# Optimization experiments

Hardware: AMD Instinct MI355X
Metric: run time of the kernel (lower is better)

## Reference

```python
import jax, jax.numpy as jnp
import numpy as np

N_NODES = 100000
N_EDGES = 1600000
IN_F = 64
HIDDEN = [64, 64, 32]


def _glorot(key, shape):
    limit = float(np.sqrt(6.0 / (shape[0] + shape[1])))
    return jax.random.uniform(key, shape, jnp.float32, -limit, limit)


def setup_inputs() -> dict:
    key = jax.random.key(0)
    ks = jax.random.split(key, 5)
    x = jax.random.normal(ks[0], (N_NODES, IN_F), jnp.float32)
    edge_index = jax.random.randint(ks[1], (2, N_EDGES), 0, N_NODES, jnp.int64)
    dims = [IN_F] + HIDDEN
    params = {}
    for i in range(len(HIDDEN)):
        params[f"W{i+1}"] = _glorot(ks[2 + i], (dims[i], dims[i + 1]))
        params[f"b{i+1}"] = jnp.zeros((dims[i + 1],), jnp.float32)
    return {"x": x, "edge_index": edge_index, **params}


def _gcn_layer(x, src, dst, norm, W, b, n):
    # PyG GCNConv: linear transform, then normalized scatter-sum aggregation, then bias
    h = x @ W                                  # [N, out]
    msg = norm[:, None] * h[src]               # gather + edge scaling, [E+N, out]
    out = jax.ops.segment_sum(msg, dst, num_segments=n)
    return out + b


def reference(x, edge_index, W1, b1, W2, b2, W3, b3):
    n = x.shape[0]
    # add self-loops (GCNConv default add_self_loops=True)
    loops = jnp.arange(n, dtype=edge_index.dtype)
    src = jnp.concatenate([edge_index[0], loops])
    dst = jnp.concatenate([edge_index[1], loops])
    # symmetric normalization: deg over destination (col), norm = d^-1/2[src]*d^-1/2[dst]
    deg = jax.ops.segment_sum(jnp.ones_like(src, x.dtype), dst, num_segments=n)
    dinv = jnp.where(deg > 0, jax.lax.rsqrt(deg), 0.0)
    norm = dinv[src] * dinv[dst]
    h = jax.nn.relu(_gcn_layer(x, src, dst, norm, W1, b1, n))
    h = jax.nn.relu(_gcn_layer(h, src, dst, norm, W2, b2, n))
    return _gcn_layer(h, src, dst, norm, W3, b3, n)
```

## Files before the change

### kernel.cpp

```cpp
#include <hip/hip_runtime.h>
#include <hip/hip_bf16.h>


#define BLOCK 256
#define NBUCKET 512
#define CHUNK 4096
#define SLOT 4608
#define MAX_NPB 256

typedef float f32x4 __attribute__((ext_vector_type(4)));

__device__ __forceinline__ float4 fma4(float s, float4 a, float4 b) {
  return make_float4(fmaf(s, a.x, b.x), fmaf(s, a.y, b.y),
                     fmaf(s, a.z, b.z), fmaf(s, a.w, b.w));
}

__device__ __forceinline__ unsigned int bf16r(float f) {
  unsigned int u = __float_as_uint(f);
  u += 0x7fffu + ((u >> 16) & 1u);
  return u >> 16;
}

__device__ __forceinline__ void acc_bf8(float4& lo, float4& hi, uint4 u) {
  lo.x += __uint_as_float(u.x << 16);
  lo.y += __uint_as_float(u.x & 0xffff0000u);
  lo.z += __uint_as_float(u.y << 16);
  lo.w += __uint_as_float(u.y & 0xffff0000u);
  hi.x += __uint_as_float(u.z << 16);
  hi.y += __uint_as_float(u.z & 0xffff0000u);
  hi.z += __uint_as_float(u.w << 16);
  hi.w += __uint_as_float(u.w & 0xffff0000u);
}


__global__ __launch_bounds__(BLOCK) void binning_kernel(
    const int* __restrict__ src, const int* __restrict__ dst,
    int* __restrict__ bcursor, int* __restrict__ binned, int e, int npb) {
  __shared__ int h[NBUCKET];
  __shared__ int base[NBUCKET];
  for (int i = threadIdx.x; i < NBUCKET; i += BLOCK) h[i] = 0;
  __syncthreads();
  const int cbase = blockIdx.x * CHUNK;
#pragma unroll
  for (int k = 0; k < CHUNK; k += BLOCK * 4) {
    int i = cbase + k + threadIdx.x * 4;
    if (i + 3 < e) {
      int4 d4 = *(const int4*)(dst + i);
      atomicAdd(&h[d4.x / npb], 1);
      atomicAdd(&h[d4.y / npb], 1);
      atomicAdd(&h[d4.z / npb], 1);
      atomicAdd(&h[d4.w / npb], 1);
    } else {
      for (int t = 0; t < 4; ++t)
        if (i + t < e) atomicAdd(&h[dst[i + t] / npb], 1);
    }
  }
  __syncthreads();
  for (int i = threadIdx.x; i < NBUCKET; i += BLOCK) {
    int c = h[i];
    base[i] = c ? atomicAdd(&bcursor[i], c) : 0;
    h[i] = 0;
  }
  __syncthreads();
#pragma unroll
  for (int k = 0; k < CHUNK; k += BLOCK * 4) {
    int i = cbase + k + threadIdx.x * 4;
    if (i + 3 < e) {
      int4 d4 = *(const int4*)(dst + i);
      int4 s4 = *(const int4*)(src + i);
      int b0 = d4.x / npb, b1 = d4.y / npb, b2 = d4.z / npb, b3 = d4.w / npb;
      int o0 = atomicAdd(&h[b0], 1);
      int o1 = atomicAdd(&h[b1], 1);
      int o2 = atomicAdd(&h[b2], 1);
      int o3 = atomicAdd(&h[b3], 1);
      binned[b0 * SLOT + base[b0] + o0] = s4.x | ((d4.x - b0 * npb) << 17);
      binned[b1 * SLOT + base[b1] + o1] = s4.y | ((d4.y - b1 * npb) << 17);
      binned[b2 * SLOT + base[b2] + o2] = s4.z | ((d4.z - b2 * npb) << 17);
      binned[b3 * SLOT + base[b3] + o3] = s4.w | ((d4.w - b3 * npb) << 17);
    } else {
      for (int t = 0; t < 4; ++t) {
        if (i + t < e) {
          int d = dst[i + t];
          int bkt = d / npb;
          int lofs = atomicAdd(&h[bkt], 1);
          binned[bkt * SLOT + base[bkt] + lofs] =
              src[i + t] | ((d - bkt * npb) << 17);
        }
      }
    }
  }
}

__global__ __launch_bounds__(BLOCK) void bucket_build(
    const int* __restrict__ binned, const int* __restrict__ bcursor,
    int* __restrict__ offs, int* __restrict__ cnt, float* __restrict__ dinv,
    int* __restrict__ csr_src, int n, int npb) {
  __shared__ int nhist[MAX_NPB];
  __shared__ int noff[MAX_NPB];
  __shared__ int lcsr[SLOT];
  const int b = blockIdx.x;
  const int node_base = b * npb;
  const int nodes = min(npb, n - node_base);
  if (nodes <= 0) return;
  const int ebase = b * SLOT;
  const int ecnt = bcursor[b];
  for (int i = threadIdx.x; i < npb; i += BLOCK) nhist[i] = 0;
  __syncthreads();
  for (int i = threadIdx.x; i < ecnt; i += BLOCK)
    atomicAdd(&nhist[binned[ebase + i] >> 17], 1);
  __syncthreads();
  if (threadIdx.x < 64) {
    const int lane = threadIdx.x;
    const int bi = lane * 4;
    int v0 = (bi + 0 < nodes) ? nhist[bi + 0] : 0;
    int v1 = (bi + 1 < nodes) ? nhist[bi + 1] : 0;
    int v2 = (bi + 2 < nodes) ? nhist[bi + 2] : 0;
    int v3 = (bi + 3 < nodes) ? nhist[bi + 3] : 0;
    int tsum = v0 + v1 + v2 + v3;
    int s = tsum;
#pragma unroll
    for (int o = 1; o < 64; o <<= 1) {
      int u = __shfl_up(s, o, 64);
      if (lane >= o) s += u;
    }
    int texcl = s - tsum;
    if (bi + 0 < nodes) noff[bi + 0] = texcl;
    if (bi + 1 < nodes) noff[bi + 1] = texcl + v0;
    if (bi + 2 < nodes) noff[bi + 2] = texcl + v0 + v1;
    if (bi + 3 < nodes) noff[bi + 3] = texcl + v0 + v1 + v2;
  }
  __syncthreads();
  for (int i = threadIdx.x; i < nodes; i += BLOCK) {
    int c = nhist[i];
    offs[node_base + i] = ebase + noff[i];
    cnt[node_base + i] = c;
    dinv[node_base + i] = rsqrtf((float)(c + 1));
  }
  __syncthreads();
  for (int i = threadIdx.x; i < ecnt; i += BLOCK) {
    int v = binned[ebase + i];
    int pos = atomicAdd(&noff[v >> 17], 1);
    lcsr[pos] = v & 0x1ffff;
  }
  __syncthreads();
  for (int i = threadIdx.x; i < ecnt; i += BLOCK)
    csr_src[ebase + i] = lcsr[i];
}


__global__ __launch_bounds__(BLOCK) void gemm1_kernel(
    const float* __restrict__ x, const float* __restrict__ W,
    const float* __restrict__ dinv, unsigned short* __restrict__ hbf, int n) {
  __shared__ float Ws[64 * 64];
  for (int i = threadIdx.x * 4; i < 64 * 64; i += BLOCK * 4)
    *(float4*)(Ws + i) = *(const float4*)(W + i);
  __syncthreads();
  const int row = blockIdx.x * 16 + (int)(threadIdx.x >> 4);
  const int c4 = (threadIdx.x & 15) * 4;
  if (row >= n) return;
  const float* xr = x + (size_t)row * 64;
  float4 acc = make_float4(0.f, 0.f, 0.f, 0.f);
#pragma unroll
  for (int k = 0; k < 64; k += 4) {
    f32x4 xn = __builtin_nontemporal_load((const f32x4*)(xr + k));
    float4 w0 = *(const float4*)(Ws + (k + 0) * 64 + c4);
    float4 w1 = *(const float4*)(Ws + (k + 1) * 64 + c4);
    float4 w2 = *(const float4*)(Ws + (k + 2) * 64 + c4);
    float4 w3 = *(const float4*)(Ws + (k + 3) * 64 + c4);
    acc = fma4(xn.x, w0, acc);
    acc = fma4(xn.y, w1, acc);
    acc = fma4(xn.z, w2, acc);
    acc = fma4(xn.w, w3, acc);
  }
  float d = dinv[row];
  uint2 packed;
  packed.x = bf16r(d * acc.x) | (bf16r(d * acc.y) << 16);
  packed.y = bf16r(d * acc.z) | (bf16r(d * acc.w) << 16);
  *(uint2*)(hbf + (size_t)row * 64 + c4) = packed;
}

template <int FOUT>
__global__ __launch_bounds__(BLOCK) void fused_agg_gemm(
    const unsigned short* __restrict__ hin, const int* __restrict__ csr_src,
    const int* __restrict__ offs, const int* __restrict__ cnt,
    const float* __restrict__ dinv, const float* __restrict__ bias,
    const float* __restrict__ Wn, unsigned short* __restrict__ hout, int n) {
  __shared__ float Ws[64 * FOUT];
  __shared__ float vrow[32][68];
  for (int i = threadIdx.x * 4; i < 64 * FOUT; i += BLOCK * 4)
    *(float4*)(Ws + i) = *(const float4*)(Wn + i);
  __syncthreads();
  const int g = threadIdx.x >> 3;
  const int lane8 = threadIdx.x & 7;
  const int c8 = lane8 * 8;
  const int node = blockIdx.x * 32 + g;
  const bool valid = node < n;
  float dnode = 0.f;
  if (valid) {
    const int start = offs[node];
    const int cn = cnt[node];
    const unsigned short* hcol = hin + c8;
    float4 l0 = make_float4(0.f, 0.f, 0.f, 0.f), h0 = l0;
    float4 l1 = l0, h1 = l0, l2 = l0, h2 = l0, l3 = l0, h3 = l0;
    acc_bf8(l0, h0, *(const uint4*)(hcol + (size_t)node * 64));
    int j = 0;
    for (; j + 4 <= cn; j += 4) {
      int s0 = csr_src[start + j + 0];
      int s1 = csr_src[start + j + 1];
      int s2 = csr_src[start + j + 2];
      int s3 = csr_src[start + j + 3];
      uint4 u0 = *(const uint4*)(hcol + (size_t)s0 * 64);
      uint4 u1 = *(const uint4*)(hcol + (size_t)s1 * 64);
      uint4 u2 = *(const uint4*)(hcol + (size_t)s2 * 64);
      uint4 u3 = *(const uint4*)(hcol + (size_t)s3 * 64);
      acc_bf8(l0, h0, u0);
      acc_bf8(l1, h1, u1);
      acc_bf8(l2, h2, u2);
      acc_bf8(l3, h3, u3);
    }
    if (j + 2 <= cn) {
      int s0 = csr_src[start + j + 0];
      int s1 = csr_src[start + j + 1];
      uint4 u0 = *(const uint4*)(hcol + (size_t)s0 * 64);
      uint4 u1 = *(const uint4*)(hcol + (size_t)s1 * 64);
      acc_bf8(l1, h1, u0);
      acc_bf8(l2, h2, u1);
      j += 2;
    }
    if (j < cn) {
      int s0 = csr_src[start + j];
      acc_bf8(l3, h3, *(const uint4*)(hcol + (size_t)s0 * 64));
    }
    float4 alo = make_float4((l0.x + l1.x) + (l2.x + l3.x),
                             (l0.y + l1.y) + (l2.y + l3.y),
                             (l0.z + l1.z) + (l2.z + l3.z),
                             (l0.w + l1.w) + (l2.w + l3.w));
    float4 ahi = make_float4((h0.x + h1.x) + (h2.x + h3.x),
                             (h0.y + h1.y) + (h2.y + h3.y),
                             (h0.z + h1.z) + (h2.z + h3.z),
                             (h0.w + h1.w) + (h2.w + h3.w));
    dnode = dinv[node];
    float4 blo = *(const float4*)(bias + c8);
    float4 bhi = *(const float4*)(bias + c8 + 4);
    float4 vlo = make_float4(fmaxf(fmaf(dnode, alo.x, blo.x), 0.f),
                             fmaxf(fmaf(dnode, alo.y, blo.y), 0.f),
                             fmaxf(fmaf(dnode, alo.z, blo.z), 0.f),
                             fmaxf(fmaf(dnode, alo.w, blo.w), 0.f));
    float4 vhi = make_float4(fmaxf(fmaf(dnode, ahi.x, bhi.x), 0.f),
                             fmaxf(fmaf(dnode, ahi.y, bhi.y), 0.f),
                             fmaxf(fmaf(dnode, ahi.z, bhi.z), 0.f),
                             fmaxf(fmaf(dnode, ahi.w, bhi.w), 0.f));
    *(float4*)(&vrow[g][c8]) = vlo;
    *(float4*)(&vrow[g][c8 + 4]) = vhi;
  }
  if (valid) {
    constexpr int CPL = FOUT / 8;
    const int cc = lane8 * CPL;
    float4 a0 = make_float4(0.f, 0.f, 0.f, 0.f);
    float4 a1 = a0;
#pragma unroll
    for (int k = 0; k < 64; k += 4) {
      float4 rv = *(const float4*)(&vrow[g][k]);
#pragma unroll
      for (int jj = 0; jj < 4; ++jj) {
        float rk = (jj == 0) ? rv.x : (jj == 1) ? rv.y : (jj == 2) ? rv.z : rv.w;
        a0 = fma4(rk, *(const float4*)(Ws + (k + jj) * FOUT + cc), a0);
        if (CPL == 8)
          a1 = fma4(rk, *(const float4*)(Ws + (k + jj) * FOUT + cc + 4), a1);
      }
    }
    if (CPL == 8) {
      uint4 packed;
      packed.x = bf16r(dnode * a0.x) | (bf16r(dnode * a0.y) << 16);
      packed.y = bf16r(dnode * a0.z) | (bf16r(dnode * a0.w) << 16);
      packed.z = bf16r(dnode * a1.x) | (bf16r(dnode * a1.y) << 16);
      packed.w = bf16r(dnode * a1.z) | (bf16r(dnode * a1.w) << 16);
      *(uint4*)(hout + (size_t)node * FOUT + cc) = packed;
    } else {
      uint2 packed;
      packed.x = bf16r(dnode * a0.x) | (bf16r(dnode * a0.y) << 16);
      packed.y = bf16r(dnode * a0.z) | (bf16r(dnode * a0.w) << 16);
      *(uint2*)(hout + (size_t)node * FOUT + cc) = packed;
    }
  }
}

__global__ __launch_bounds__(BLOCK) void agg3_kernel(
    const unsigned short* __restrict__ hbf, const int* __restrict__ csr_src,
    const int* __restrict__ offs, const int* __restrict__ cnt,
    const float* __restrict__ dinv, const float* __restrict__ bias,
    float* __restrict__ out, int n) {
  constexpr int F = 32;
  const int node = blockIdx.x * 64 + (int)(threadIdx.x >> 2);
  const int c8 = (threadIdx.x & 3) * 8;
  if (node >= n) return;
  const int start = offs[node];
  const int cn = cnt[node];
  const unsigned short* hcol = hbf + c8;
  float4 l0 = make_float4(0.f, 0.f, 0.f, 0.f), h0 = l0;
  float4 l1 = l0, h1 = l0, l2 = l0, h2 = l0, l3 = l0, h3 = l0;
  acc_bf8(l0, h0, *(const uint4*)(hcol + (size_t)node * F));
  int j = 0;
  for (; j + 4 <= cn; j += 4) {
    int s0 = csr_src[start + j + 0];
    int s1 = csr_src[start + j + 1];
    int s2 = csr_src[start + j + 2];
    int s3 = csr_src[start + j + 3];
    uint4 u0 = *(const uint4*)(hcol + (size_t)s0 * F);
    uint4 u1 = *(const uint4*)(hcol + (size_t)s1 * F);
    uint4 u2 = *(const uint4*)(hcol + (size_t)s2 * F);
    uint4 u3 = *(const uint4*)(hcol + (size_t)s3 * F);
    acc_bf8(l0, h0, u0);
    acc_bf8(l1, h1, u1);
    acc_bf8(l2, h2, u2);
    acc_bf8(l3, h3, u3);
  }
  if (j + 2 <= cn) {
    int s0 = csr_src[start + j + 0];
    int s1 = csr_src[start + j + 1];
    uint4 u0 = *(const uint4*)(hcol + (size_t)s0 * F);
    uint4 u1 = *(const uint4*)(hcol + (size_t)s1 * F);
    acc_bf8(l1, h1, u0);
    acc_bf8(l2, h2, u1);
    j += 2;
  }
  if (j < cn) {
    int s0 = csr_src[start + j];
    acc_bf8(l3, h3, *(const uint4*)(hcol + (size_t)s0 * F));
  }
  float4 alo = make_float4((l0.x + l1.x) + (l2.x + l3.x),
                           (l0.y + l1.y) + (l2.y + l3.y),
                           (l0.z + l1.z) + (l2.z + l3.z),
                           (l0.w + l1.w) + (l2.w + l3.w));
  float4 ahi = make_float4((h0.x + h1.x) + (h2.x + h3.x),
                           (h0.y + h1.y) + (h2.y + h3.y),
                           (h0.z + h1.z) + (h2.z + h3.z),
                           (h0.w + h1.w) + (h2.w + h3.w));
  float d = dinv[node];
  float4 blo = *(const float4*)(bias + c8);
  float4 bhi = *(const float4*)(bias + c8 + 4);
  f32x4 vlo = {fmaf(d, alo.x, blo.x), fmaf(d, alo.y, blo.y),
               fmaf(d, alo.z, blo.z), fmaf(d, alo.w, blo.w)};
  f32x4 vhi = {fmaf(d, ahi.x, bhi.x), fmaf(d, ahi.y, bhi.y),
               fmaf(d, ahi.z, bhi.z), fmaf(d, ahi.w, bhi.w)};
  float* op = out + (size_t)node * F + c8;
  __builtin_nontemporal_store(vlo, (f32x4*)op);
  __builtin_nontemporal_store(vhi, (f32x4*)(op + 4));
}

static inline size_t align_up(size_t v, size_t a) { return (v + a - 1) & ~(a - 1); }

extern "C" void kernel_launch(void* const* d_in, const int* in_sizes, int n_in,
                              void* d_out, int out_size, void* d_ws, size_t ws_size,
                              hipStream_t stream) {
  const float* x = (const float*)d_in[0];
  const int* edge_index = (const int*)d_in[1];
  const float* W1 = (const float*)d_in[2];
  const float* b1 = (const float*)d_in[3];
  const float* W2 = (const float*)d_in[4];
  const float* b2 = (const float*)d_in[5];
  const float* W3 = (const float*)d_in[6];
  const float* b3 = (const float*)d_in[7];
  float* out = (float*)d_out;

  const int n = in_sizes[0] / 64;
  const int e = in_sizes[1] / 2;
  const int* e_src = edge_index;
  const int* e_dst = edge_index + e;
  const int npb = (n + NBUCKET - 1) / NBUCKET;

  char* ws = (char*)d_ws;
  size_t off = 0;
  int* bcursor = (int*)(ws + off); off = align_up(off + NBUCKET * 4, 512);
  int* offs    = (int*)(ws + off); off = align_up(off + (size_t)n * 4, 512);
  int* cnt     = (int*)(ws + off); off = align_up(off + (size_t)n * 4, 512);
  float* dinv  = (float*)(ws + off); off = align_up(off + (size_t)n * 4, 512);
  int* binned  = (int*)(ws + off); off = align_up(off + (size_t)NBUCKET * SLOT * 4, 512);
  int* csr_src = (int*)(ws + off); off = align_up(off + (size_t)NBUCKET * SLOT * 4, 512);
  unsigned short* hbuf_a = (unsigned short*)(ws + off);
  off = align_up(off + (size_t)n * 64 * 2, 512);
  unsigned short* hbuf_b = (unsigned short*)(ws + off);
  off = align_up(off + (size_t)n * 64 * 2, 512);
  (void)ws_size;

  const int gC = (e + CHUNK - 1) / CHUNK;

  hipMemsetAsync(bcursor, 0, NBUCKET * 4, stream);
  binning_kernel<<<gC, BLOCK, 0, stream>>>(e_src, e_dst, bcursor, binned, e, npb);
  bucket_build<<<NBUCKET, BLOCK, 0, stream>>>(binned, bcursor, offs, cnt, dinv,
                                              csr_src, n, npb);

  gemm1_kernel<<<(n + 15) / 16, BLOCK, 0, stream>>>(x, W1, dinv, hbuf_a, n);
  fused_agg_gemm<64><<<(n + 31) / 32, BLOCK, 0, stream>>>(
      hbuf_a, csr_src, offs, cnt, dinv, b1, W2, hbuf_b, n);
  fused_agg_gemm<32><<<(n + 31) / 32, BLOCK, 0, stream>>>(
      hbuf_b, csr_src, offs, cnt, dinv, b2, W3, hbuf_a, n);
  agg3_kernel<<<(n + 63) / 64, BLOCK, 0, stream>>>(hbuf_a, csr_src, offs, cnt,
                                                   dinv, b3, out, n);
}
```

Measured before the change: 252.1 us.

## Split each node's neighbor gather across two thread halves with shuffle reduction

The fused aggregation+GEMM kernels and the final aggregation kernel now give each node twice as many threads. The two halves take alternating 4-edge chunks of the neighbor list, and their partial sums are combined with an xor shuffle. The small per-node GEMM is re-split across 16 lanes, and grids are doubled. This aims to expose more memory-level parallelism in the latency-bound gathers (about 16 neighbors per node), at the cost of more threads per node, extra shuffles and idle lanes in the epilogue.

```diff
diff --git a/kernel.cpp b/kernel.cpp
--- a/kernel.cpp
+++ b/kernel.cpp
@@ -186,14 +186,16 @@
     const float* __restrict__ dinv, const float* __restrict__ bias,
     const float* __restrict__ Wn, unsigned short* __restrict__ hout, int n) {
   __shared__ float Ws[64 * FOUT];
-  __shared__ float vrow[32][68];
+  __shared__ float vrow[16][68];
   for (int i = threadIdx.x * 4; i < 64 * FOUT; i += BLOCK * 4)
     *(float4*)(Ws + i) = *(const float4*)(Wn + i);
   __syncthreads();
-  const int g = threadIdx.x >> 3;
-  const int lane8 = threadIdx.x & 7;
-  const int c8 = lane8 * 8;
-  const int node = blockIdx.x * 32 + g;
+  const int g = threadIdx.x >> 4;
+  const int lane16 = threadIdx.x & 15;
+  const int colgrp = lane16 & 7;
+  const int half = lane16 >> 3;
+  const int c8 = colgrp * 8;
+  const int node = blockIdx.x * 16 + g;
   const bool valid = node < n;
   float dnode = 0.f;
   if (valid) {
@@ -202,9 +204,10 @@
     const unsigned short* hcol = hin + c8;
     float4 l0 = make_float4(0.f, 0.f, 0.f, 0.f), h0 = l0;
     float4 l1 = l0, h1 = l0, l2 = l0, h2 = l0, l3 = l0, h3 = l0;
-    acc_bf8(l0, h0, *(const uint4*)(hcol + (size_t)node * 64));
-    int j = 0;
-    for (; j + 4 <= cn; j += 4) {
+    if (half == 0)
+      acc_bf8(l0, h0, *(const uint4*)(hcol + (size_t)node * 64));
+    int j = half * 4;
+    for (; j + 4 <= cn; j += 8) {
       int s0 = csr_src[start + j + 0];
       int s1 = csr_src[start + j + 1];
       int s2 = csr_src[start + j + 2];
@@ -218,18 +221,18 @@
       acc_bf8(l2, h2, u2);
       acc_bf8(l3, h3, u3);
     }
-    if (j + 2 <= cn) {
-      int s0 = csr_src[start + j + 0];
-      int s1 = csr_src[start + j + 1];
-      uint4 u0 = *(const uint4*)(hcol + (size_t)s0 * 64);
-      uint4 u1 = *(const uint4*)(hcol + (size_t)s1 * 64);
-      acc_bf8(l1, h1, u0);
-      acc_bf8(l2, h2, u1);
-      j += 2;
-    }
     if (j < cn) {
+      int rem = cn - j;
       int s0 = csr_src[start + j];
-      acc_bf8(l3, h3, *(const uint4*)(hcol + (size_t)s0 * 64));
+      acc_bf8(l1, h1, *(const uint4*)(hcol + (size_t)s0 * 64));
+      if (rem > 1) {
+        int s1 = csr_src[start + j + 1];
+        acc_bf8(l2, h2, *(const uint4*)(hcol + (size_t)s1 * 64));
+      }
+      if (rem > 2) {
+        int s2 = csr_src[start + j + 2];
+        acc_bf8(l3, h3, *(const uint4*)(hcol + (size_t)s2 * 64));
+      }
     }
     float4 alo = make_float4((l0.x + l1.x) + (l2.x + l3.x),
                              (l0.y + l1.y) + (l2.y + l3.y),
@@ -239,48 +242,59 @@
                              (h0.y + h1.y) + (h2.y + h3.y),
                              (h0.z + h1.z) + (h2.z + h3.z),
                              (h0.w + h1.w) + (h2.w + h3.w));
+    alo.x += __shfl_xor(alo.x, 8); alo.y += __shfl_xor(alo.y, 8);
+    alo.z += __shfl_xor(alo.z, 8); alo.w += __shfl_xor(alo.w, 8);
+    ahi.x += __shfl_xor(ahi.x, 8); ahi.y += __shfl_xor(ahi.y, 8);
+    ahi.z += __shfl_xor(ahi.z, 8); ahi.w += __shfl_xor(ahi.w, 8);
     dnode = dinv[node];
-    float4 blo = *(const float4*)(bias + c8);
-    float4 bhi = *(const float4*)(bias + c8 + 4);
-    float4 vlo = make_float4(fmaxf(fmaf(dnode, alo.x, blo.x), 0.f),
-                             fmaxf(fmaf(dnode, alo.y, blo.y), 0.f),
-                             fmaxf(fmaf(dnode, alo.z, blo.z), 0.f),
-                             fmaxf(fmaf(dnode, alo.w, blo.w), 0.f));
-    float4 vhi = make_float4(fmaxf(fmaf(dnode, ahi.x, bhi.x), 0.f),
-                             fmaxf(fmaf(dnode, ahi.y, bhi.y), 0.f),
-                             fmaxf(fmaf(dnode, ahi.z, bhi.z), 0.f),
-                             fmaxf(fmaf(dnode, ahi.w, bhi.w), 0.f));
-    *(float4*)(&vrow[g][c8]) = vlo;
-    *(float4*)(&vrow[g][c8 + 4]) = vhi;
+    if (half == 0) {
+      float4 blo = *(const float4*)(bias + c8);
+      float4 bhi = *(const float4*)(bias + c8 + 4);
+      float4 vlo = make_float4(fmaxf(fmaf(dnode, alo.x, blo.x), 0.f),
+                               fmaxf(fmaf(dnode, alo.y, blo.y), 0.f),
+                               fmaxf(fmaf(dnode, alo.z, blo.z), 0.f),
+                               fmaxf(fmaf(dnode, alo.w, blo.w), 0.f));
+      float4 vhi = make_float4(fmaxf(fmaf(dnode, ahi.x, bhi.x), 0.f),
+                               fmaxf(fmaf(dnode, ahi.y, bhi.y), 0.f),
+                               fmaxf(fmaf(dnode, ahi.z, bhi.z), 0.f),
+                               fmaxf(fmaf(dnode, ahi.w, bhi.w), 0.f));
+      *(float4*)(&vrow[g][c8]) = vlo;
+      *(float4*)(&vrow[g][c8 + 4]) = vhi;
+    }
   }
   if (valid) {
-    constexpr int CPL = FOUT / 8;
-    const int cc = lane8 * CPL;
-    float4 a0 = make_float4(0.f, 0.f, 0.f, 0.f);
-    float4 a1 = a0;
-#pragma unroll
-    for (int k = 0; k < 64; k += 4) {
-      float4 rv = *(const float4*)(&vrow[g][k]);
-#pragma unroll
-      for (int jj = 0; jj < 4; ++jj) {
-        float rk = (jj == 0) ? rv.x : (jj == 1) ? rv.y : (jj == 2) ? rv.z : rv.w;
-        a0 = fma4(rk, *(const float4*)(Ws + (k + jj) * FOUT + cc), a0);
-        if (CPL == 8)
-          a1 = fma4(rk, *(const float4*)(Ws + (k + jj) * FOUT + cc + 4), a1);
+    if (FOUT == 64) {
+      const int cc = lane16 * 4;
+      float4 a0 = make_float4(0.f, 0.f, 0.f, 0.f);
+#pragma unroll
+      for (int k = 0; k < 64; k += 4) {
+        float4 rv = *(const float4*)(&vrow[g][k]);
+        a0 = fma4(rv.x, *(const float4*)(Ws + (k + 0) * 64 + cc), a0);
+        a0 = fma4(rv.y, *(const float4*)(Ws + (k + 1) * 64 + cc), a0);
+        a0 = fma4(rv.z, *(const float4*)(Ws + (k + 2) * 64 + cc), a0);
+        a0 = fma4(rv.w, *(const float4*)(Ws + (k + 3) * 64 + cc), a0);
       }
-    }
-    if (CPL == 8) {
-      uint4 packed;
-      packed.x = bf16r(dnode * a0.x) | (bf16r(dnode * a0.y) << 16);
-      packed.y = bf16r(dnode * a0.z) | (bf16r(dnode * a0.w) << 16);
-      packed.z = bf16r(dnode * a1.x) | (bf16r(dnode * a1.y) << 16);
-      packed.w = bf16r(dnode * a1.z) | (bf16r(dnode * a1.w) << 16);
-      *(uint4*)(hout + (size_t)node * FOUT + cc) = packed;
-    } else {
       uint2 packed;
       packed.x = bf16r(dnode * a0.x) | (bf16r(dnode * a0.y) << 16);
       packed.y = bf16r(dnode * a0.z) | (bf16r(dnode * a0.w) << 16);
-      *(uint2*)(hout + (size_t)node * FOUT + cc) = packed;
+      *(uint2*)(hout + (size_t)node * 64 + cc) = packed;
+    } else {
+      const int cc = lane16 * 2;
+      float ax = 0.f, ay = 0.f;
+#pragma unroll
+      for (int k = 0; k < 64; k += 4) {
+        float4 rv = *(const float4*)(&vrow[g][k]);
+        ax = fmaf(rv.x, Ws[(k + 0) * 32 + cc + 0], ax);
+        ay = fmaf(rv.x, Ws[(k + 0) * 32 + cc + 1], ay);
+        ax = fmaf(rv.y, Ws[(k + 1) * 32 + cc + 0], ax);
+        ay = fmaf(rv.y, Ws[(k + 1) * 32 + cc + 1], ay);
+        ax = fmaf(rv.z, Ws[(k + 2) * 32 + cc + 0], ax);
+        ay = fmaf(rv.z, Ws[(k + 2) * 32 + cc + 1], ay);
+        ax = fmaf(rv.w, Ws[(k + 3) * 32 + cc + 0], ax);
+        ay = fmaf(rv.w, Ws[(k + 3) * 32 + cc + 1], ay);
+      }
+      unsigned int packed = bf16r(dnode * ax) | (bf16r(dnode * ay) << 16);
+      *(unsigned int*)(hout + (size_t)node * 32 + cc) = packed;
     }
   }
 }
@@ -291,17 +305,21 @@
     const float* __restrict__ dinv, const float* __restrict__ bias,
     float* __restrict__ out, int n) {
   constexpr int F = 32;
-  const int node = blockIdx.x * 64 + (int)(threadIdx.x >> 2);
-  const int c8 = (threadIdx.x & 3) * 8;
+  const int g = threadIdx.x >> 3;
+  const int lane8 = threadIdx.x & 7;
+  const int colgrp = lane8 & 3;
+  const int half = lane8 >> 2;
+  const int c8 = colgrp * 8;
+  const int node = blockIdx.x * 32 + g;
   if (node >= n) return;
   const int start = offs[node];
   const int cn = cnt[node];
   const unsigned short* hcol = hbf + c8;
   float4 l0 = make_float4(0.f, 0.f, 0.f, 0.f), h0 = l0;
   float4 l1 = l0, h1 = l0, l2 = l0, h2 = l0, l3 = l0, h3 = l0;
-  acc_bf8(l0, h0, *(const uint4*)(hcol + (size_t)node * F));
-  int j = 0;
-  for (; j + 4 <= cn; j += 4) {
+  if (half == 0) acc_bf8(l0, h0, *(const uint4*)(hcol + (size_t)node * F));
+  int j = half * 4;
+  for (; j + 4 <= cn; j += 8) {
     int s0 = csr_src[start + j + 0];
     int s1 = csr_src[start + j + 1];
     int s2 = csr_src[start + j + 2];
@@ -315,18 +333,18 @@
     acc_bf8(l2, h2, u2);
     acc_bf8(l3, h3, u3);
   }
-  if (j + 2 <= cn) {
-    int s0 = csr_src[start + j + 0];
-    int s1 = csr_src[start + j + 1];
-    uint4 u0 = *(const uint4*)(hcol + (size_t)s0 * F);
-    uint4 u1 = *(const uint4*)(hcol + (size_t)s1 * F);
-    acc_bf8(l1, h1, u0);
-    acc_bf8(l2, h2, u1);
-    j += 2;
-  }
   if (j < cn) {
+    int rem = cn - j;
     int s0 = csr_src[start + j];
-    acc_bf8(l3, h3, *(const uint4*)(hcol + (size_t)s0 * F));
+    acc_bf8(l1, h1, *(const uint4*)(hcol + (size_t)s0 * F));
+    if (rem > 1) {
+      int s1 = csr_src[start + j + 1];
+      acc_bf8(l2, h2, *(const uint4*)(hcol + (size_t)s1 * F));
+    }
+    if (rem > 2) {
+      int s2 = csr_src[start + j + 2];
+      acc_bf8(l3, h3, *(const uint4*)(hcol + (size_t)s2 * F));
+    }
   }
   float4 alo = make_float4((l0.x + l1.x) + (l2.x + l3.x),
                            (l0.y + l1.y) + (l2.y + l3.y),
@@ -336,6 +354,11 @@
                            (h0.y + h1.y) + (h2.y + h3.y),
                            (h0.z + h1.z) + (h2.z + h3.z),
                            (h0.w + h1.w) + (h2.w + h3.w));
+  alo.x += __shfl_xor(alo.x, 4); alo.y += __shfl_xor(alo.y, 4);
+  alo.z += __shfl_xor(alo.z, 4); alo.w += __shfl_xor(alo.w, 4);
+  ahi.x += __shfl_xor(ahi.x, 4); ahi.y += __shfl_xor(ahi.y, 4);
+  ahi.z += __shfl_xor(ahi.z, 4); ahi.w += __shfl_xor(ahi.w, 4);
+  if (half != 0) return;
   float d = dinv[node];
   float4 blo = *(const float4*)(bias + c8);
   float4 bhi = *(const float4*)(bias + c8 + 4);
@@ -391,10 +414,10 @@
                                               csr_src, n, npb);
 
   gemm1_kernel<<<(n + 15) / 16, BLOCK, 0, stream>>>(x, W1, dinv, hbuf_a, n);
-  fused_agg_gemm<64><<<(n + 31) / 32, BLOCK, 0, stream>>>(
+  fused_agg_gemm<64><<<(n + 15) / 16, BLOCK, 0, stream>>>(
       hbuf_a, csr_src, offs, cnt, dinv, b1, W2, hbuf_b, n);
-  fused_agg_gemm<32><<<(n + 31) / 32, BLOCK, 0, stream>>>(
+  fused_agg_gemm<32><<<(n + 15) / 16, BLOCK, 0, stream>>>(
       hbuf_b, csr_src, offs, cnt, dinv, b2, W3, hbuf_a, n);
-  agg3_kernel<<<(n + 63) / 64, BLOCK, 0, stream>>>(hbuf_a, csr_src, offs, cnt,
+  agg3_kernel<<<(n + 31) / 32, BLOCK, 0, stream>>>(hbuf_a, csr_src, offs, cnt,
                                                    dinv, b3, out, n);
 }
```

Result: slower. 260.4 us (+3.3%).

## Split features into column-slab layout and unfuse aggregation from the dense transforms

Applied to the files above, without the earlier changes.

Features are now stored in planar slabs of 8 (or 16) bf16 columns per node, so each aggregation thread gathers one 16-byte slab per neighbor. The slab index is interleaved across blocks so that concurrently resident work touches a smaller, more cache-resident working set. The fused aggregate-then-GEMM kernels become separate aggregation kernels (bias, ReLU, bf16 output) and standalone GEMMs that compute two rows per thread. This trades extra kernel launches and an extra round trip of intermediate activations through memory for better gather locality and simpler kernels.

```diff
diff --git a/kernel.cpp b/kernel.cpp
--- a/kernel.cpp
+++ b/kernel.cpp
@@ -150,166 +150,142 @@
 
 __global__ __launch_bounds__(BLOCK) void gemm1_kernel(
     const float* __restrict__ x, const float* __restrict__ W,
-    const float* __restrict__ dinv, unsigned short* __restrict__ hbf, int n) {
+    const float* __restrict__ dinv, unsigned short* __restrict__ hout, int n) {
   __shared__ float Ws[64 * 64];
   for (int i = threadIdx.x * 4; i < 64 * 64; i += BLOCK * 4)
     *(float4*)(Ws + i) = *(const float4*)(W + i);
   __syncthreads();
-  const int row = blockIdx.x * 16 + (int)(threadIdx.x >> 4);
-  const int c4 = (threadIdx.x & 15) * 4;
-  if (row >= n) return;
-  const float* xr = x + (size_t)row * 64;
-  float4 acc = make_float4(0.f, 0.f, 0.f, 0.f);
+  const int cg = threadIdx.x & 7;
+  const int rloc = threadIdx.x >> 3;
+  const int r0 = blockIdx.x * 64 + rloc;
+  const int r1 = r0 + 32;
+  const int rc0 = min(r0, n - 1), rc1 = min(r1, n - 1);
+  float4 a00 = make_float4(0.f, 0.f, 0.f, 0.f);
+  float4 a01 = a00, a10 = a00, a11 = a00;
+  const int c8 = cg * 8;
 #pragma unroll
   for (int k = 0; k < 64; k += 4) {
-    f32x4 xn = __builtin_nontemporal_load((const f32x4*)(xr + k));
-    float4 w0 = *(const float4*)(Ws + (k + 0) * 64 + c4);
-    float4 w1 = *(const float4*)(Ws + (k + 1) * 64 + c4);
-    float4 w2 = *(const float4*)(Ws + (k + 2) * 64 + c4);
-    float4 w3 = *(const float4*)(Ws + (k + 3) * 64 + c4);
-    acc = fma4(xn.x, w0, acc);
-    acc = fma4(xn.y, w1, acc);
-    acc = fma4(xn.z, w2, acc);
-    acc = fma4(xn.w, w3, acc);
-  }
-  float d = dinv[row];
-  uint2 packed;
-  packed.x = bf16r(d * acc.x) | (bf16r(d * acc.y) << 16);
-  packed.y = bf16r(d * acc.z) | (bf16r(d * acc.w) << 16);
-  *(uint2*)(hbf + (size_t)row * 64 + c4) = packed;
+    float4 x0 = *(const float4*)(x + (size_t)rc0 * 64 + k);
+    float4 x1 = *(const float4*)(x + (size_t)rc1 * 64 + k);
+#pragma unroll
+    for (int kk = 0; kk < 4; ++kk) {
+      float4 w0 = *(const float4*)(Ws + (k + kk) * 64 + c8);
+      float4 w1 = *(const float4*)(Ws + (k + kk) * 64 + c8 + 4);
+      float s0 = (kk == 0) ? x0.x : (kk == 1) ? x0.y : (kk == 2) ? x0.z : x0.w;
+      float s1 = (kk == 0) ? x1.x : (kk == 1) ? x1.y : (kk == 2) ? x1.z : x1.w;
+      a00 = fma4(s0, w0, a00);
+      a01 = fma4(s0, w1, a01);
+      a10 = fma4(s1, w0, a10);
+      a11 = fma4(s1, w1, a11);
+    }
+  }
+  const size_t pstride = (size_t)n * 8;
+  if (r0 < n) {
+    float d = dinv[r0];
+    uint4 p;
+    p.x = bf16r(d * a00.x) | (bf16r(d * a00.y) << 16);
+    p.y = bf16r(d * a00.z) | (bf16r(d * a00.w) << 16);
+    p.z = bf16r(d * a01.x) | (bf16r(d * a01.y) << 16);
+    p.w = bf16r(d * a01.z) | (bf16r(d * a01.w) << 16);
+    *(uint4*)(hout + cg * pstride + (size_t)r0 * 8) = p;
+  }
+  if (r1 < n) {
+    float d = dinv[r1];
+    uint4 p;
+    p.x = bf16r(d * a10.x) | (bf16r(d * a10.y) << 16);
+    p.y = bf16r(d * a10.z) | (bf16r(d * a10.w) << 16);
+    p.z = bf16r(d * a11.x) | (bf16r(d * a11.y) << 16);
+    p.w = bf16r(d * a11.z) | (bf16r(d * a11.w) << 16);
+    *(uint4*)(hout + cg * pstride + (size_t)r1 * 8) = p;
+  }
 }
 
 template <int FOUT>
-__global__ __launch_bounds__(BLOCK) void fused_agg_gemm(
+__global__ __launch_bounds__(BLOCK) void gemmB_kernel(
+    const unsigned short* __restrict__ ain, const float* __restrict__ W,
+    const float* __restrict__ dinv, unsigned short* __restrict__ hout, int n) {
+  __shared__ float Ws[64 * FOUT];
+  for (int i = threadIdx.x * 4; i < 64 * FOUT; i += BLOCK * 4)
+    *(float4*)(Ws + i) = *(const float4*)(W + i);
+  __syncthreads();
+  constexpr int CG = FOUT / 8;
+  constexpr int RPB = 2 * (BLOCK / CG);
+  const int cg = threadIdx.x & (CG - 1);
+  const int rloc = threadIdx.x / CG;
+  const int r0 = blockIdx.x * RPB + rloc;
+  const int r1 = r0 + RPB / 2;
+  const int rc0 = min(r0, n - 1), rc1 = min(r1, n - 1);
+  const size_t pin = (size_t)n * 8;
+  float4 a00 = make_float4(0.f, 0.f, 0.f, 0.f);
+  float4 a01 = a00, a10 = a00, a11 = a00;
+  const int c8 = cg * 8;
+#pragma unroll
+  for (int p = 0; p < 8; ++p) {
+    uint4 u0 = *(const uint4*)(ain + p * pin + (size_t)rc0 * 8);
+    uint4 u1 = *(const uint4*)(ain + p * pin + (size_t)rc1 * 8);
+    float x0[8], x1[8];
+    x0[0] = __uint_as_float(u0.x << 16); x0[1] = __uint_as_float(u0.x & 0xffff0000u);
+    x0[2] = __uint_as_float(u0.y << 16); x0[3] = __uint_as_float(u0.y & 0xffff0000u);
+    x0[4] = __uint_as_float(u0.z << 16); x0[5] = __uint_as_float(u0.z & 0xffff0000u);
+    x0[6] = __uint_as_float(u0.w << 16); x0[7] = __uint_as_float(u0.w & 0xffff0000u);
+    x1[0] = __uint_as_float(u1.x << 16); x1[1] = __uint_as_float(u1.x & 0xffff0000u);
+    x1[2] = __uint_as_float(u1.y << 16); x1[3] = __uint_as_float(u1.y & 0xffff0000u);
+    x1[4] = __uint_as_float(u1.z << 16); x1[5] = __uint_as_float(u1.z & 0xffff0000u);
+    x1[6] = __uint_as_float(u1.w << 16); x1[7] = __uint_as_float(u1.w & 0xffff0000u);
+#pragma unroll
+    for (int kk = 0; kk < 8; ++kk) {
+      const int k = p * 8 + kk;
+      float4 w0 = *(const float4*)(Ws + k * FOUT + c8);
+      float4 w1 = *(const float4*)(Ws + k * FOUT + c8 + 4);
+      a00 = fma4(x0[kk], w0, a00);
+      a01 = fma4(x0[kk], w1, a01);
+      a10 = fma4(x1[kk], w0, a10);
+      a11 = fma4(x1[kk], w1, a11);
+    }
+  }
+  auto store = [&](int r, float4 lo, float4 hi) {
+    float d = dinv[r];
+    uint4 p;
+    p.x = bf16r(d * lo.x) | (bf16r(d * lo.y) << 16);
+    p.y = bf16r(d * lo.z) | (bf16r(d * lo.w) << 16);
+    p.z = bf16r(d * hi.x) | (bf16r(d * hi.y) << 16);
+    p.w = bf16r(d * hi.z) | (bf16r(d * hi.w) << 16);
+    if (FOUT == 64) {
+      *(uint4*)(hout + cg * ((size_t)n * 8) + (size_t)r * 8) = p;
+    } else {
+      *(uint4*)(hout + (cg >> 1) * ((size_t)n * 16) + (size_t)r * 16 +
+                (cg & 1) * 8) = p;
+    }
+  };
+  if (r0 < n) store(r0, a00, a01);
+  if (r1 < n) store(r1, a10, a11);
+}
+
+
+__global__ __launch_bounds__(BLOCK) void agg8_kernel(
     const unsigned short* __restrict__ hin, const int* __restrict__ csr_src,
     const int* __restrict__ offs, const int* __restrict__ cnt,
     const float* __restrict__ dinv, const float* __restrict__ bias,
-    const float* __restrict__ Wn, unsigned short* __restrict__ hout, int n) {
-  __shared__ float Ws[64 * FOUT];
-  __shared__ float vrow[32][68];
-  for (int i = threadIdx.x * 4; i < 64 * FOUT; i += BLOCK * 4)
-    *(float4*)(Ws + i) = *(const float4*)(Wn + i);
-  __syncthreads();
-  const int g = threadIdx.x >> 3;
-  const int lane8 = threadIdx.x & 7;
-  const int c8 = lane8 * 8;
-  const int node = blockIdx.x * 32 + g;
-  const bool valid = node < n;
-  float dnode = 0.f;
-  if (valid) {
-    const int start = offs[node];
-    const int cn = cnt[node];
-    const unsigned short* hcol = hin + c8;
-    float4 l0 = make_float4(0.f, 0.f, 0.f, 0.f), h0 = l0;
-    float4 l1 = l0, h1 = l0, l2 = l0, h2 = l0, l3 = l0, h3 = l0;
-    acc_bf8(l0, h0, *(const uint4*)(hcol + (size_t)node * 64));
-    int j = 0;
-    for (; j + 4 <= cn; j += 4) {
-      int s0 = csr_src[start + j + 0];
-      int s1 = csr_src[start + j + 1];
-      int s2 = csr_src[start + j + 2];
-      int s3 = csr_src[start + j + 3];
-      uint4 u0 = *(const uint4*)(hcol + (size_t)s0 * 64);
-      uint4 u1 = *(const uint4*)(hcol + (size_t)s1 * 64);
-      uint4 u2 = *(const uint4*)(hcol + (size_t)s2 * 64);
-      uint4 u3 = *(const uint4*)(hcol + (size_t)s3 * 64);
-      acc_bf8(l0, h0, u0);
-      acc_bf8(l1, h1, u1);
-      acc_bf8(l2, h2, u2);
-      acc_bf8(l3, h3, u3);
-    }
-    if (j + 2 <= cn) {
-      int s0 = csr_src[start + j + 0];
-      int s1 = csr_src[start + j + 1];
-      uint4 u0 = *(const uint4*)(hcol + (size_t)s0 * 64);
-      uint4 u1 = *(const uint4*)(hcol + (size_t)s1 * 64);
-      acc_bf8(l1, h1, u0);
-      acc_bf8(l2, h2, u1);
-      j += 2;
-    }
-    if (j < cn) {
-      int s0 = csr_src[start + j];
-      acc_bf8(l3, h3, *(const uint4*)(hcol + (size_t)s0 * 64));
-    }
-    float4 alo = make_float4((l0.x + l1.x) + (l2.x + l3.x),
-                             (l0.y + l1.y) + (l2.y + l3.y),
-                             (l0.z + l1.z) + (l2.z + l3.z),
-                             (l0.w + l1.w) + (l2.w + l3.w));
-    float4 ahi = make_float4((h0.x + h1.x) + (h2.x + h3.x),
-                             (h0.y + h1.y) + (h2.y + h3.y),
-                             (h0.z + h1.z) + (h2.z + h3.z),
-                             (h0.w + h1.w) + (h2.w + h3.w));
-    dnode = dinv[node];
-    float4 blo = *(const float4*)(bias + c8);
-    float4 bhi = *(const float4*)(bias + c8 + 4);
-    float4 vlo = make_float4(fmaxf(fmaf(dnode, alo.x, blo.x), 0.f),
-                             fmaxf(fmaf(dnode, alo.y, blo.y), 0.f),
-                             fmaxf(fmaf(dnode, alo.z, blo.z), 0.f),
-                             fmaxf(fmaf(dnode, alo.w, blo.w), 0.f));
-    float4 vhi = make_float4(fmaxf(fmaf(dnode, ahi.x, bhi.x), 0.f),
-                             fmaxf(fmaf(dnode, ahi.y, bhi.y), 0.f),
-                             fmaxf(fmaf(dnode, ahi.z, bhi.z), 0.f),
-                             fmaxf(fmaf(dnode, ahi.w, bhi.w), 0.f));
-    *(float4*)(&vrow[g][c8]) = vlo;
-    *(float4*)(&vrow[g][c8 + 4]) = vhi;
-  }
-  if (valid) {
-    constexpr int CPL = FOUT / 8;
-    const int cc = lane8 * CPL;
-    float4 a0 = make_float4(0.f, 0.f, 0.f, 0.f);
-    float4 a1 = a0;
-#pragma unroll
-    for (int k = 0; k < 64; k += 4) {
-      float4 rv = *(const float4*)(&vrow[g][k]);
-#pragma unroll
-      for (int jj = 0; jj < 4; ++jj) {
-        float rk = (jj == 0) ? rv.x : (jj == 1) ? rv.y : (jj == 2) ? rv.z : rv.w;
-        a0 = fma4(rk, *(const float4*)(Ws + (k + jj) * FOUT + cc), a0);
-        if (CPL == 8)
-          a1 = fma4(rk, *(const float4*)(Ws + (k + jj) * FOUT + cc + 4), a1);
-      }
-    }
-    if (CPL == 8) {
-      uint4 packed;
-      packed.x = bf16r(dnode * a0.x) | (bf16r(dnode * a0.y) << 16);
-      packed.y = bf16r(dnode * a0.z) | (bf16r(dnode * a0.w) << 16);
-      packed.z = bf16r(dnode * a1.x) | (bf16r(dnode * a1.y) << 16);
-      packed.w = bf16r(dnode * a1.z) | (bf16r(dnode * a1.w) << 16);
-      *(uint4*)(hout + (size_t)node * FOUT + cc) = packed;
-    } else {
-      uint2 packed;
-      packed.x = bf16r(dnode * a0.x) | (bf16r(dnode * a0.y) << 16);
-      packed.y = bf16r(dnode * a0.z) | (bf16r(dnode * a0.w) << 16);
-      *(uint2*)(hout + (size_t)node * FOUT + cc) = packed;
-    }
-  }
-}
-
-__global__ __launch_bounds__(BLOCK) void agg3_kernel(
-    const unsigned short* __restrict__ hbf, const int* __restrict__ csr_src,
-    const int* __restrict__ offs, const int* __restrict__ cnt,
-    const float* __restrict__ dinv, const float* __restrict__ bias,
-    float* __restrict__ out, int n) {
-  constexpr int F = 32;
-  const int node = blockIdx.x * 64 + (int)(threadIdx.x >> 2);
-  const int c8 = (threadIdx.x & 3) * 8;
+    unsigned short* __restrict__ aout, int n) {
+  const int s = blockIdx.x & 7;
+  const int node = (blockIdx.x >> 3) * BLOCK + threadIdx.x;
   if (node >= n) return;
+  const unsigned short* hp = hin + (size_t)s * n * 8;
   const int start = offs[node];
   const int cn = cnt[node];
-  const unsigned short* hcol = hbf + c8;
   float4 l0 = make_float4(0.f, 0.f, 0.f, 0.f), h0 = l0;
   float4 l1 = l0, h1 = l0, l2 = l0, h2 = l0, l3 = l0, h3 = l0;
-  acc_bf8(l0, h0, *(const uint4*)(hcol + (size_t)node * F));
+  acc_bf8(l0, h0, *(const uint4*)(hp + (size_t)node * 8));
   int j = 0;
   for (; j + 4 <= cn; j += 4) {
     int s0 = csr_src[start + j + 0];
     int s1 = csr_src[start + j + 1];
     int s2 = csr_src[start + j + 2];
     int s3 = csr_src[start + j + 3];
-    uint4 u0 = *(const uint4*)(hcol + (size_t)s0 * F);
-    uint4 u1 = *(const uint4*)(hcol + (size_t)s1 * F);
-    uint4 u2 = *(const uint4*)(hcol + (size_t)s2 * F);
-    uint4 u3 = *(const uint4*)(hcol + (size_t)s3 * F);
+    uint4 u0 = *(const uint4*)(hp + (size_t)s0 * 8);
+    uint4 u1 = *(const uint4*)(hp + (size_t)s1 * 8);
+    uint4 u2 = *(const uint4*)(hp + (size_t)s2 * 8);
+    uint4 u3 = *(const uint4*)(hp + (size_t)s3 * 8);
     acc_bf8(l0, h0, u0);
     acc_bf8(l1, h1, u1);
     acc_bf8(l2, h2, u2);
@@ -318,15 +294,15 @@
   if (j + 2 <= cn) {
     int s0 = csr_src[start + j + 0];
     int s1 = csr_src[start + j + 1];
-    uint4 u0 = *(const uint4*)(hcol + (size_t)s0 * F);
-    uint4 u1 = *(const uint4*)(hcol + (size_t)s1 * F);
+    uint4 u0 = *(const uint4*)(hp + (size_t)s0 * 8);
+    uint4 u1 = *(const uint4*)(hp + (size_t)s1 * 8);
     acc_bf8(l1, h1, u0);
     acc_bf8(l2, h2, u1);
     j += 2;
   }
   if (j < cn) {
     int s0 = csr_src[start + j];
-    acc_bf8(l3, h3, *(const uint4*)(hcol + (size_t)s0 * F));
+    acc_bf8(l3, h3, *(const uint4*)(hp + (size_t)s0 * 8));
   }
   float4 alo = make_float4((l0.x + l1.x) + (l2.x + l3.x),
                            (l0.y + l1.y) + (l2.y + l3.y),
@@ -337,15 +313,79 @@
                            (h0.z + h1.z) + (h2.z + h3.z),
                            (h0.w + h1.w) + (h2.w + h3.w));
   float d = dinv[node];
-  float4 blo = *(const float4*)(bias + c8);
-  float4 bhi = *(const float4*)(bias + c8 + 4);
-  f32x4 vlo = {fmaf(d, alo.x, blo.x), fmaf(d, alo.y, blo.y),
-               fmaf(d, alo.z, blo.z), fmaf(d, alo.w, blo.w)};
-  f32x4 vhi = {fmaf(d, ahi.x, bhi.x), fmaf(d, ahi.y, bhi.y),
-               fmaf(d, ahi.z, bhi.z), fmaf(d, ahi.w, bhi.w)};
-  float* op = out + (size_t)node * F + c8;
-  __builtin_nontemporal_store(vlo, (f32x4*)op);
-  __builtin_nontemporal_store(vhi, (f32x4*)(op + 4));
+  float4 blo = *(const float4*)(bias + s * 8);
+  float4 bhi = *(const float4*)(bias + s * 8 + 4);
+  uint4 p;
+  p.x = bf16r(fmaxf(fmaf(d, alo.x, blo.x), 0.f)) |
+        (bf16r(fmaxf(fmaf(d, alo.y, blo.y), 0.f)) << 16);
+  p.y = bf16r(fmaxf(fmaf(d, alo.z, blo.z), 0.f)) |
+        (bf16r(fmaxf(fmaf(d, alo.w, blo.w), 0.f)) << 16);
+  p.z = bf16r(fmaxf(fmaf(d, ahi.x, bhi.x), 0.f)) |
+        (bf16r(fmaxf(fmaf(d, ahi.y, bhi.y), 0.f)) << 16);
+  p.w = bf16r(fmaxf(fmaf(d, ahi.z, bhi.z), 0.f)) |
+        (bf16r(fmaxf(fmaf(d, ahi.w, bhi.w), 0.f)) << 16);
+  *(uint4*)(aout + (size_t)s * n * 8 + (size_t)node * 8) = p;
+}
+
+__global__ __launch_bounds__(BLOCK) void agg16f_kernel(
+    const unsigned short* __restrict__ hin, const int* __restrict__ csr_src,
+    const int* __restrict__ offs, const int* __restrict__ cnt,
+    const float* __restrict__ dinv, const float* __restrict__ bias,
+    float* __restrict__ out, int n) {
+  const int s = blockIdx.x & 1;
+  const int node = (blockIdx.x >> 1) * BLOCK + threadIdx.x;
+  if (node >= n) return;
+  const unsigned short* hp = hin + (size_t)s * n * 16;
+  const int start = offs[node];
+  const int cn = cnt[node];
+  float4 al0 = make_float4(0.f, 0.f, 0.f, 0.f), ah0 = al0;
+  float4 bl0 = al0, bh0 = al0;
+  float4 al1 = al0, ah1 = al0, bl1 = al0, bh1 = al0;
+  {
+    uint4 u0 = *(const uint4*)(hp + (size_t)node * 16);
+    uint4 u1 = *(const uint4*)(hp + (size_t)node * 16 + 8);
+    acc_bf8(al0, ah0, u0);
+    acc_bf8(bl0, bh0, u1);
+  }
+  int j = 0;
+  for (; j + 2 <= cn; j += 2) {
+    int s0 = csr_src[start + j + 0];
+    int s1 = csr_src[start + j + 1];
+    uint4 u00 = *(const uint4*)(hp + (size_t)s0 * 16);
+    uint4 u01 = *(const uint4*)(hp + (size_t)s0 * 16 + 8);
+    uint4 u10 = *(const uint4*)(hp + (size_t)s1 * 16);
+    uint4 u11 = *(const uint4*)(hp + (size_t)s1 * 16 + 8);
+    acc_bf8(al0, ah0, u00);
+    acc_bf8(bl0, bh0, u01);
+    acc_bf8(al1, ah1, u10);
+    acc_bf8(bl1, bh1, u11);
+  }
+  if (j < cn) {
+    int s0 = csr_src[start + j];
+    uint4 u0 = *(const uint4*)(hp + (size_t)s0 * 16);
+    uint4 u1 = *(const uint4*)(hp + (size_t)s0 * 16 + 8);
+    acc_bf8(al1, ah1, u0);
+    acc_bf8(bl1, bh1, u1);
+  }
+  float4 A = make_float4(al0.x + al1.x, al0.y + al1.y, al0.z + al1.z, al0.w + al1.w);
+  float4 B = make_float4(ah0.x + ah1.x, ah0.y + ah1.y, ah0.z + ah1.z, ah0.w + ah1.w);
+  float4 C = make_float4(bl0.x + bl1.x, bl0.y + bl1.y, bl0.z + bl1.z, bl0.w + bl1.w);
+  float4 D = make_float4(bh0.x + bh1.x, bh0.y + bh1.y, bh0.z + bh1.z, bh0.w + bh1.w);
+  float d = dinv[node];
+  const float* bp = bias + s * 16;
+  float4 b0 = *(const float4*)(bp);
+  float4 b1 = *(const float4*)(bp + 4);
+  float4 b2 = *(const float4*)(bp + 8);
+  float4 b3 = *(const float4*)(bp + 12);
+  f32x4 v0 = {fmaf(d, A.x, b0.x), fmaf(d, A.y, b0.y), fmaf(d, A.z, b0.z), fmaf(d, A.w, b0.w)};
+  f32x4 v1 = {fmaf(d, B.x, b1.x), fmaf(d, B.y, b1.y), fmaf(d, B.z, b1.z), fmaf(d, B.w, b1.w)};
+  f32x4 v2 = {fmaf(d, C.x, b2.x), fmaf(d, C.y, b2.y), fmaf(d, C.z, b2.z), fmaf(d, C.w, b2.w)};
+  f32x4 v3 = {fmaf(d, D.x, b3.x), fmaf(d, D.y, b3.y), fmaf(d, D.z, b3.z), fmaf(d, D.w, b3.w)};
+  float* op = out + (size_t)node * 32 + s * 16;
+  __builtin_nontemporal_store(v0, (f32x4*)op);
+  __builtin_nontemporal_store(v1, (f32x4*)(op + 4));
+  __builtin_nontemporal_store(v2, (f32x4*)(op + 8));
+  __builtin_nontemporal_store(v3, (f32x4*)(op + 12));
 }
 
 static inline size_t align_up(size_t v, size_t a) { return (v + a - 1) & ~(a - 1); }
@@ -377,24 +417,29 @@
   float* dinv  = (float*)(ws + off); off = align_up(off + (size_t)n * 4, 512);
   int* binned  = (int*)(ws + off); off = align_up(off + (size_t)NBUCKET * SLOT * 4, 512);
   int* csr_src = (int*)(ws + off); off = align_up(off + (size_t)NBUCKET * SLOT * 4, 512);
-  unsigned short* hbuf_a = (unsigned short*)(ws + off);
+  unsigned short* hbuf = (unsigned short*)(ws + off);
   off = align_up(off + (size_t)n * 64 * 2, 512);
-  unsigned short* hbuf_b = (unsigned short*)(ws + off);
+  unsigned short* abuf = (unsigned short*)(ws + off);
   off = align_up(off + (size_t)n * 64 * 2, 512);
+  unsigned short* h3buf = (unsigned short*)(ws + off);
+  off = align_up(off + (size_t)n * 32 * 2, 512);
   (void)ws_size;
 
   const int gC = (e + CHUNK - 1) / CHUNK;
+  const int ntile = (n + BLOCK - 1) / BLOCK;
 
   hipMemsetAsync(bcursor, 0, NBUCKET * 4, stream);
   binning_kernel<<<gC, BLOCK, 0, stream>>>(e_src, e_dst, bcursor, binned, e, npb);
   bucket_build<<<NBUCKET, BLOCK, 0, stream>>>(binned, bcursor, offs, cnt, dinv,
                                               csr_src, n, npb);
 
-  gemm1_kernel<<<(n + 15) / 16, BLOCK, 0, stream>>>(x, W1, dinv, hbuf_a, n);
-  fused_agg_gemm<64><<<(n + 31) / 32, BLOCK, 0, stream>>>(
-      hbuf_a, csr_src, offs, cnt, dinv, b1, W2, hbuf_b, n);
-  fused_agg_gemm<32><<<(n + 31) / 32, BLOCK, 0, stream>>>(
-      hbuf_b, csr_src, offs, cnt, dinv, b2, W3, hbuf_a, n);
-  agg3_kernel<<<(n + 63) / 64, BLOCK, 0, stream>>>(hbuf_a, csr_src, offs, cnt,
-                                                   dinv, b3, out, n);
-}
+  gemm1_kernel<<<(n + 63) / 64, BLOCK, 0, stream>>>(x, W1, dinv, hbuf, n);
+  agg8_kernel<<<ntile * 8, BLOCK, 0, stream>>>(hbuf, csr_src, offs, cnt, dinv,
+                                               b1, abuf, n);
+  gemmB_kernel<64><<<(n + 63) / 64, BLOCK, 0, stream>>>(abuf, W2, dinv, hbuf, n);
+  agg8_kernel<<<ntile * 8, BLOCK, 0, stream>>>(hbuf, csr_src, offs, cnt, dinv,
+                                               b2, abuf, n);
+  gemmB_kernel<32><<<(n + 127) / 128, BLOCK, 0, stream>>>(abuf, W3, dinv, h3buf, n);
+  agg16f_kernel<<<ntile * 2, BLOCK, 0, stream>>>(h3buf, csr_src, offs, cnt,
+                                                 dinv, b3, out, n);
+}
```

Result: slower. 980.3 us (+288.8%).
